# Kernel tuning notes

Hardware: AMD Instinct MI355X
Metric: run time of the kernel (lower is better)

## Reference

```python
import jax, jax.numpy as jnp
import numpy as np
from jax import lax

STRIDE, PAD, K = 1, 1, 3  # module defaults


def setup_inputs() -> dict:
    key = jax.random.key(0)
    k1, k2, k3, k4 = jax.random.split(key, 4)
    N, C, H, W, O = 8, 64, 112, 112, 64
    n = K * K
    x = jax.random.normal(k1, (N, C, H, W), jnp.float32)
    # kaiming-uniform-ish scale for main conv weight
    weight = jax.random.normal(k2, (O, C, K, K), jnp.float32) * (1.0 / np.sqrt(C * K * K))
    bias = jnp.zeros((O,), jnp.float32)
    # small random offset predictor (original zero-inits; small values exercise bilinear path)
    offset_w = jax.random.normal(k3, (3 * n, C, K, K), jnp.float32) * 0.01
    offset_b = jax.random.normal(k4, (3 * n,), jnp.float32) * 0.01
    return {"x": x, "weight": weight, "bias": bias, "offset_w": offset_w, "offset_b": offset_b}


def _bilinear(x, py, px):
    """Zero-padded bilinear sampling. x:[N,C,H,W]; py,px:[N,n,Ho,Wo] -> [N,C,n,Ho,Wo]."""
    N, C, H, W = x.shape
    xf = x.reshape(N, C, H * W)
    y0 = jnp.floor(py)
    x0 = jnp.floor(px)
    out = jnp.zeros((N, C) + py.shape[1:], x.dtype)
    for dy in (0.0, 1.0):
        for dx in (0.0, 1.0):
            yi = y0 + dy
            xi = x0 + dx
            w = (1.0 - jnp.abs(py - yi)) * (1.0 - jnp.abs(px - xi))
            valid = (yi >= 0) & (yi <= H - 1) & (xi >= 0) & (xi <= W - 1)
            yc = jnp.clip(yi, 0, H - 1).astype(jnp.int32)
            xc = jnp.clip(xi, 0, W - 1).astype(jnp.int32)
            idx = (yc * W + xc).reshape(N, 1, -1)
            g = jnp.take_along_axis(xf, jnp.broadcast_to(idx, (N, C, idx.shape[-1])), axis=2)
            g = g.reshape((N, C) + py.shape[1:])
            out = out + g * jnp.where(valid, w, 0.0)[:, None]
    return out


def reference(x, weight, bias, offset_w, offset_b):
    N, C, H, W = x.shape
    O = weight.shape[0]
    n = K * K
    # offset/mask predictor: 3x3 conv -> [N, 3*n, Ho, Wo]
    raw = lax.conv_general_dilated(
        x, offset_w, (STRIDE, STRIDE), [(PAD, PAD), (PAD, PAD)],
        dimension_numbers=("NCHW", "OIHW", "NCHW"),
    ) + offset_b[None, :, None, None]
    Ho, Wo = raw.shape[2], raw.shape[3]
    off = raw[:, : 2 * n].reshape(N, n, 2, Ho, Wo)       # (dy, dx) per tap
    mask = jax.nn.sigmoid(raw[:, 2 * n :])               # [N, n, Ho, Wo]
    # base sampling grid: p0 + kernel tap position
    tap_y = (jnp.arange(n) // K).astype(jnp.float32)[:, None, None]   # [n,1,1]
    tap_x = (jnp.arange(n) % K).astype(jnp.float32)[:, None, None]
    base_y = (jnp.arange(Ho) * STRIDE - PAD).astype(jnp.float32)[None, :, None] + tap_y  # [n,Ho,1]
    base_x = (jnp.arange(Wo) * STRIDE - PAD).astype(jnp.float32)[None, None, :] + tap_x  # [n,1,Wo]
    py = off[:, :, 0] + base_y[None]   # [N,n,Ho,Wo]
    px = off[:, :, 1] + base_x[None]
    sampled = _bilinear(x, py, px)                       # [N,C,n,Ho,Wo]
    val = sampled * mask[:, None]                        # modulation
    out = jnp.einsum("ncthw,oct->nohw", val, weight.reshape(O, C, n))
    return out + bias[None, :, None, None]
```

## Files before the change

kernel.cpp:

```cpp
#include <hip/hip_runtime.h>
#include <hip/hip_fp16.h>
#include <math.h>

#define NB  8
#define CIN 64
#define HH  112
#define WW  112
#define OC  64
#define HWSZ (HH*WW)
#define NPOS (NB*HWSZ)

#define PR 9
#define PC 21
#define NPOSP (PR*PC)
#define PATCH_CHUNKS (NPOSP*8)

#define TP_BLOCKS (HWSZ/64*NB)

typedef unsigned short u16;
typedef __attribute__((ext_vector_type(8))) _Float16 h8;
typedef __attribute__((ext_vector_type(4))) float floatx4;

#define XT_ELEMS   (NB*HWSZ*CIN)
#define WSWZ_ELEMS (18*4*64*8)
#define OSWZ_ELEMS (18*4*32*8)

union CV { uint4 u; h8 h; };

__device__ __forceinline__ u16 f2h(float f) { return __half_as_ushort(__float2half(f)); }
__device__ __forceinline__ __half2 H2(unsigned v) { union { unsigned u; __half2 h; } c; c.u = v; return c.h; }
__device__ __forceinline__ unsigned U2(__half2 h) { union { unsigned u; __half2 h; } c; c.h = h; return c.u; }
__device__ __forceinline__ unsigned pkh(float lo, float hi) {
    union { __half2 h; unsigned u; } c;
    c.h = __floats2half2_rn(lo, hi);
    return c.u;
}

struct TapW { __half2 w00, w01, w10, w11; };

__global__ __launch_bounds__(256) void prep_k(
    const float* __restrict__ x, const float* __restrict__ wgt,
    const float* __restrict__ offw,
    u16* __restrict__ xt, u16* __restrict__ wswz, u16* __restrict__ oswz)
{
    __shared__ float t[64][65];
    const int tid = threadIdx.x;
    const int bid = blockIdx.x;
    if (bid < TP_BLOCKS) {
        const int n   = bid & 7;
        const int hw0 = (bid >> 3) * 64;
        const int wv  = tid & 63;
        const int g   = tid >> 6;
        #pragma unroll
        for (int i = 0; i < 16; ++i) {
            const int c = i*4 + g;
            t[c][wv] = x[((size_t)n*CIN + c)*HWSZ + hw0 + wv];
        }
        __syncthreads();
        #pragma unroll
        for (int i = 0; i < 4; ++i) {
            const int unit = i*256 + tid;
            const int cg = unit & 15;
            const int hw = unit >> 4;
            uint2 o;
            o.x = pkh(t[cg*4+0][hw], t[cg*4+1][hw]);
            o.y = pkh(t[cg*4+2][hw], t[cg*4+3][hw]);
            *(uint2*)(xt + ((size_t)n*HWSZ + hw0 + hw)*CIN + cg*4) = o;
        }
    } else {
        const int gid = (bid - TP_BLOCKS)*256 + tid;
        if (gid < WSWZ_ELEMS) {
            const int j = gid & 7, o = (gid >> 3) & 63, q = (gid >> 9) & 3, s = gid >> 11;
            const int k = s*32 + q*8 + j;
            const int c = k & 63, tt = k >> 6;
            wswz[gid] = f2h(wgt[o*576 + c*9 + tt]);
        } else {
            const int g2 = gid - WSWZ_ELEMS;
            const int j = g2 & 7, r = (g2 >> 3) & 31, q = (g2 >> 8) & 3, s = g2 >> 10;
            const int k = s*32 + q*8 + j;
            const int c = k & 63, tt = k >> 6;
            oswz[g2] = (r < 27) ? f2h(offw[r*576 + c*9 + tt]) : (u16)0;
        }
    }
}

#define IML(DST, S_) { \
    const int t_ = (S_) >> 1; \
    const int ty_ = t_/3, tx_ = t_ - 3*ty_; \
    const int r_ = wid + 1 + ty_; \
    const int c_ = m + 1 + tx_; \
    const int pos_ = r_*PC + c_; \
    const int ck_ = ((S_) & 1)*4 + q; \
    DST = *(const uint4*)(patch + pos_*128 + ((ck_ ^ (pos_ & 7)) << 4)); }

#define OFF_MFMA(SRC, S_) { CV cb_; cb_.u = (SRC); \
    const u16* ap_ = oswz + ((S_)*4 + q)*256 + m*8; \
    acc0 = __builtin_amdgcn_mfma_f32_16x16x32_f16(*(const h8*)(ap_),       cb_.h, acc0, 0, 0, 0); \
    acc1 = __builtin_amdgcn_mfma_f32_16x16x32_f16(*(const h8*)(ap_ + 128), cb_.h, acc1, 0, 0, 0); }

#define HALF_STEP(R00, R01, R10, R11, TW, S_) { \
    CV cb_; \
    cb_.u.x = U2(__hfma2(H2((R00).x),(TW).w00, __hfma2(H2((R01).x),(TW).w01, \
              __hfma2(H2((R10).x),(TW).w10, __hmul2(H2((R11).x),(TW).w11))))); \
    cb_.u.y = U2(__hfma2(H2((R00).y),(TW).w00, __hfma2(H2((R01).y),(TW).w01, \
              __hfma2(H2((R10).y),(TW).w10, __hmul2(H2((R11).y),(TW).w11))))); \
    cb_.u.z = U2(__hfma2(H2((R00).z),(TW).w00, __hfma2(H2((R01).z),(TW).w01, \
              __hfma2(H2((R10).z),(TW).w10, __hmul2(H2((R11).z),(TW).w11))))); \
    cb_.u.w = U2(__hfma2(H2((R00).w),(TW).w00, __hfma2(H2((R01).w),(TW).w01, \
              __hfma2(H2((R10).w),(TW).w10, __hmul2(H2((R11).w),(TW).w11))))); \
    const u16* wp_ = wswz + ((S_)*4 + q)*512 + m*8; \
    acc[0] = __builtin_amdgcn_mfma_f32_16x16x32_f16(*(const h8*)(wp_),       cb_.h, acc[0], 0, 0, 0); \
    acc[1] = __builtin_amdgcn_mfma_f32_16x16x32_f16(*(const h8*)(wp_ + 128), cb_.h, acc[1], 0, 0, 0); \
    acc[2] = __builtin_amdgcn_mfma_f32_16x16x32_f16(*(const h8*)(wp_ + 256), cb_.h, acc[2], 0, 0, 0); \
    acc[3] = __builtin_amdgcn_mfma_f32_16x16x32_f16(*(const h8*)(wp_ + 384), cb_.h, acc[3], 0, 0, 0); }

#define UNPACK_TW(TW, WX, WY) { \
    (TW).w00 = __half2half2(__ushort_as_half((u16)((WX) & 0xFFFFu))); \
    (TW).w01 = __half2half2(__ushort_as_half((u16)((WX) >> 16))); \
    (TW).w10 = __half2half2(__ushort_as_half((u16)((WY) & 0xFFFFu))); \
    (TW).w11 = __half2half2(__ushort_as_half((u16)((WY) >> 16))); }

__global__ __launch_bounds__(256)
__attribute__((amdgpu_waves_per_eu(5, 8)))
void dcn_k(
    const u16*  __restrict__ xt,
    const u16*  __restrict__ wswz,
    const u16*  __restrict__ oswz,
    const float* __restrict__ bias,
    const float* __restrict__ offb,
    float* __restrict__ out)
{
    __shared__ uint4 patch4[PATCH_CHUNKS];
    __shared__ float rawsm[4][32][16];
    char* patch = (char*)patch4;
    unsigned* prmO = (unsigned*)rawsm;
    uint2*    prmW = (uint2*)((char*)rawsm + 2304);

    const int tid  = threadIdx.x;
    const int lane = tid & 63;
    const int wid  = tid >> 6;
    const int m    = lane & 15;
    const int q    = lane >> 4;

    const int n   = blockIdx.x & 7;
    const int idx = blockIdx.x >> 3;
    const int rg  = idx / 7;
    const int cc  = idx - rg*7;
    const int hoB = rg * 4;
    const int wo0 = cc * 16;
    const int ho  = hoB + wid;
    const u16* xtn = xt + (size_t)n * HWSZ * CIN;

    #pragma unroll
    for (int i = 0; i < 6; ++i) {
        const int u = i*256 + tid;
        if (u < PATCH_CHUNKS) {
            const int pos = u >> 3, ck = u & 7;
            const int pry = pos / PC;
            const int pcx = pos - pry*PC;
            const int gy = hoB - 2 + pry;
            const int gx = wo0 - 2 + pcx;
            uint4 v = {0u,0u,0u,0u};
            if (((unsigned)gy < HH) && ((unsigned)gx < WW))
                v = *(const uint4*)(xtn + (gy*WW + gx)*CIN + ck*8);
            *(uint4*)(patch + pos*128 + ((ck ^ (pos & 7)) << 4)) = v;
        }
    }
    __syncthreads();

    {
        uint4 b[6];
        floatx4 acc0 = {0.f,0.f,0.f,0.f}, acc1 = {0.f,0.f,0.f,0.f};
        #pragma unroll
        for (int s = 0; s < 6; ++s) IML(b[s], s)
        #pragma unroll
        for (int s = 0; s < 6; ++s) {
            uint4 nv; IML(nv, s + 6)
            OFF_MFMA(b[s], s)
            b[s] = nv;
        }
        #pragma unroll
        for (int s = 0; s < 6; ++s) {
            uint4 nv; IML(nv, s + 12)
            OFF_MFMA(b[s], s + 6)
            b[s] = nv;
        }
        #pragma unroll
        for (int s = 0; s < 6; ++s) OFF_MFMA(b[s], s + 12)

        #pragma unroll
        for (int r = 0; r < 4; ++r) {
            rawsm[wid][q*4 + r][m]      = acc0[r];
            rawsm[wid][16 + q*4 + r][m] = acc1[r];
        }
    }
    __syncthreads();

    float vy[3], vx[3], vmk[3];
    #pragma unroll
    for (int i = 0; i < 3; ++i) {
        const int e = i*64 + lane;
        if (e < 144) {
            const int t = e >> 4, p = e & 15;
            vy[i]  = rawsm[wid][2*t][p];
            vx[i]  = rawsm[wid][2*t + 1][p];
            vmk[i] = rawsm[wid][18 + t][p];
        }
    }
    __syncthreads();
    #pragma unroll
    for (int i = 0; i < 3; ++i) {
        const int e = i*64 + lane;
        if (e < 144) {
            const int t = e >> 4;
            const int p = e & 15;
            const int ty = t / 3, tx = t - 3*ty;
            const float py = vy[i] + offb[2*t]     + (float)(ho - 1 + ty);
            const float px = vx[i] + offb[2*t + 1] + (float)(wo0 + p - 1 + tx);
            const float mk = 1.f / (1.f + expf(-(vmk[i] + offb[18 + t])));
            const float y0f = floorf(py), x0f = floorf(px);
            const float fy = py - y0f, fx = px - x0f;
            const int y0 = (int)y0f, x0 = (int)x0f;
            const float gy = 1.f - fy, gx = 1.f - fx;
            const bool vy0 = (unsigned)y0       < HH;
            const bool vy1 = (unsigned)(y0 + 1) < HH;
            const bool vx0 = (unsigned)x0       < WW;
            const bool vx1 = (unsigned)(x0 + 1) < WW;
            const float w00 = (vy0 && vx0) ? gy*gx*mk : 0.f;
            const float w01 = (vy0 && vx1) ? gy*fx*mk : 0.f;
            const float w10 = (vy1 && vx0) ? fy*gx*mk : 0.f;
            const float w11 = (vy1 && vx1) ? fy*fx*mk : 0.f;
            const int yc0 = min(max(y0, 0), HH-1),  yc1 = min(max(y0+1, 0), HH-1);
            const int xc0 = min(max(x0, 0), WW-1),  xc1 = min(max(x0+1, 0), WW-1);
            const unsigned o00 = (unsigned)((yc0*WW + xc0)*CIN);
            const unsigned dxb = (unsigned)(xc1 - xc0);
            const unsigned dyb = (unsigned)(yc1 - yc0);
            const int r0  = yc0 - (hoB - 2);
            const int c0l = xc0 - (wo0 - 2);
            const bool inp = (r0 >= 0) && (r0 + (int)dyb <= PR-1)
                          && (c0l >= 0) && (c0l + (int)dxb <= PC-1);
            const int pos00 = r0*PC + c0l;
            prmO[(wid*9 + t)*16 + p] = o00 | (dxb << 20) | (dyb << 21)
                            | (((unsigned)pos00 & 0xFFu) << 22)
                            | (inp ? (1u << 30) : 0u);
            uint2 Wv;
            Wv.x = (unsigned)__half_as_ushort(__float2half(w00))
                 | ((unsigned)__half_as_ushort(__float2half(w01)) << 16);
            Wv.y = (unsigned)__half_as_ushort(__float2half(w10))
                 | ((unsigned)__half_as_ushort(__float2half(w11)) << 16);
            prmW[(wid*9 + t)*16 + p] = Wv;
        }
    }
    __syncthreads();

    floatx4 acc[4];
    #pragma unroll
    for (int i = 0; i < 4; ++i) acc[i] = (floatx4){0.f,0.f,0.f,0.f};

    const unsigned* PoB = prmO + wid*144 + m;
    const uint2*    PwB = prmW + wid*144 + m;

    unsigned band = 0xFFFFFFFFu;
    #pragma unroll
    for (int t = 0; t < 9; ++t) band &= PoB[t*16];

    if (__all((int)((band >> 30) & 1u))) {
        unsigned Po = PoB[0];
        uint2    Pw = PwB[0];
        #pragma unroll
        for (int t = 0; t < 9; ++t) {
            const unsigned PoN = (t < 8) ? PoB[(t+1)*16] : 0u;
            const uint2    PwN = (t < 8) ? PwB[(t+1)*16] : Pw;
            const int p00 = (int)((Po >> 22) & 0xFFu);
            const int dxb = (int)((Po >> 20) & 1u);
            const int dyb = (int)((Po >> 21) & 1u);
            const int p01 = p00 + dxb;
            const int p10 = p00 + dyb*PC;
            const int p11 = p10 + dxb;
            const int a00 = p00*128 + ((q ^ (p00 & 7)) << 4);
            const int a01 = p01*128 + ((q ^ (p01 & 7)) << 4);
            const int a10 = p10*128 + ((q ^ (p10 & 7)) << 4);
            const int a11 = p11*128 + ((q ^ (p11 & 7)) << 4);
            const uint4 g0 = *(const uint4*)(patch + a00);
            const uint4 g1 = *(const uint4*)(patch + a01);
            const uint4 g2 = *(const uint4*)(patch + a10);
            const uint4 g3 = *(const uint4*)(patch + a11);
            const uint4 g4 = *(const uint4*)(patch + (a00 ^ 64));
            const uint4 g5 = *(const uint4*)(patch + (a01 ^ 64));
            const uint4 g6 = *(const uint4*)(patch + (a10 ^ 64));
            const uint4 g7 = *(const uint4*)(patch + (a11 ^ 64));
            TapW tw; UNPACK_TW(tw, Pw.x, Pw.y)
            HALF_STEP(g0, g1, g2, g3, tw, 2*t)
            HALF_STEP(g4, g5, g6, g7, tw, 2*t + 1)
            Po = PoN; Pw = PwN;
        }
    } else {
        const int ch0 = q*8, ch1 = 32 + q*8;
        #pragma unroll
        for (int t = 0; t < 9; ++t) {
            const unsigned Po = PoB[t*16];
            const uint2    Pw = PwB[t*16];
            TapW tw; UNPACK_TW(tw, Pw.x, Pw.y)
            uint4 g0,g1,g2,g3,g4,g5,g6,g7;
            if (__all((int)((Po >> 30) & 1u))) {
                const int p00 = (int)((Po >> 22) & 0xFFu);
                const int dxb = (int)((Po >> 20) & 1u);
                const int dyb = (int)((Po >> 21) & 1u);
                const int p01 = p00 + dxb;
                const int p10 = p00 + dyb*PC;
                const int p11 = p10 + dxb;
                const int a00 = p00*128 + ((q ^ (p00 & 7)) << 4);
                const int a01 = p01*128 + ((q ^ (p01 & 7)) << 4);
                const int a10 = p10*128 + ((q ^ (p10 & 7)) << 4);
                const int a11 = p11*128 + ((q ^ (p11 & 7)) << 4);
                g0 = *(const uint4*)(patch + a00);
                g1 = *(const uint4*)(patch + a01);
                g2 = *(const uint4*)(patch + a10);
                g3 = *(const uint4*)(patch + a11);
                g4 = *(const uint4*)(patch + (a00 ^ 64));
                g5 = *(const uint4*)(patch + (a01 ^ 64));
                g6 = *(const uint4*)(patch + (a10 ^ 64));
                g7 = *(const uint4*)(patch + (a11 ^ 64));
            } else {
                const int o00 = (int)(Po & 0xFFFFFu);
                const int dx  = (int)((Po >> 20) & 1u) << 6;
                const int dy  = (int)((Po >> 21) & 1u) * (WW*CIN);
                g0 = *(const uint4*)(xtn + o00 + ch0);
                g1 = *(const uint4*)(xtn + o00 + dx + ch0);
                g2 = *(const uint4*)(xtn + o00 + dy + ch0);
                g3 = *(const uint4*)(xtn + o00 + dx + dy + ch0);
                g4 = *(const uint4*)(xtn + o00 + ch1);
                g5 = *(const uint4*)(xtn + o00 + dx + ch1);
                g6 = *(const uint4*)(xtn + o00 + dy + ch1);
                g7 = *(const uint4*)(xtn + o00 + dx + dy + ch1);
            }
            HALF_STEP(g0, g1, g2, g3, tw, 2*t)
            HALF_STEP(g4, g5, g6, g7, tw, 2*t + 1)
        }
    }

    #pragma unroll
    for (int ob = 0; ob < 4; ++ob) {
        #pragma unroll
        for (int r = 0; r < 4; ++r) {
            const int o = ob*16 + q*4 + r;
            out[(((size_t)n*OC + o)*HH + ho)*WW + wo0 + m] = acc[ob][r] + bias[o];
        }
    }
}

extern "C" void kernel_launch(void* const* d_in, const int* in_sizes, int n_in,
                              void* d_out, int out_size, void* d_ws, size_t ws_size,
                              hipStream_t stream)
{
    const float* x    = (const float*)d_in[0];
    const float* wgt  = (const float*)d_in[1];
    const float* bias = (const float*)d_in[2];
    const float* offw = (const float*)d_in[3];
    const float* offb = (const float*)d_in[4];
    float* out = (float*)d_out;

    u16* xt   = (u16*)d_ws;
    u16* wswz = xt + XT_ELEMS;
    u16* oswz = wswz + WSWZ_ELEMS;

    prep_k<<<dim3(TP_BLOCKS + (WSWZ_ELEMS + OSWZ_ELEMS)/256), 256, 0, stream>>>(
        x, wgt, offw, xt, wswz, oswz);
    dcn_k<<<dim3(NPOS/64), 256, 0, stream>>>(xt, wswz, oswz, bias, offb, out);
}
```

Measured before the change: 115.2 us.

## Split channel reduction across two wave groups with 512-thread blocks

```diff
diff --git a/kernel.cpp b/kernel.cpp
--- a/kernel.cpp
+++ b/kernel.cpp
@@ -87,7 +87,7 @@
 #define IML(DST, S_) { \
     const int t_ = (S_) >> 1; \
     const int ty_ = t_/3, tx_ = t_ - 3*ty_; \
-    const int r_ = wid + 1 + ty_; \
+    const int r_ = row + 1 + ty_; \
     const int c_ = m + 1 + tx_; \
     const int pos_ = r_*PC + c_; \
     const int ck_ = ((S_) & 1)*4 + q; \
@@ -120,8 +120,8 @@
     (TW).w10 = __half2half2(__ushort_as_half((u16)((WY) & 0xFFFFu))); \
     (TW).w11 = __half2half2(__ushort_as_half((u16)((WY) >> 16))); }
 
-__global__ __launch_bounds__(256)
-__attribute__((amdgpu_waves_per_eu(5, 8)))
+__global__ __launch_bounds__(512)
+__attribute__((amdgpu_waves_per_eu(8)))
 void dcn_k(
     const u16*  __restrict__ xt,
     const u16*  __restrict__ wswz,
@@ -132,13 +132,15 @@
 {
     __shared__ uint4 patch4[PATCH_CHUNKS];
     __shared__ float rawsm[4][32][16];
+    __shared__ unsigned prmO[4][9][16];
+    __shared__ uint2    prmW[4][9][16];
     char* patch = (char*)patch4;
-    unsigned* prmO = (unsigned*)rawsm;
-    uint2*    prmW = (uint2*)((char*)rawsm + 2304);
 
     const int tid  = threadIdx.x;
     const int lane = tid & 63;
     const int wid  = tid >> 6;
+    const int row  = wid & 3;
+    const int h    = wid >> 2;
     const int m    = lane & 15;
     const int q    = lane >> 4;
 
@@ -148,12 +150,12 @@
     const int cc  = idx - rg*7;
     const int hoB = rg * 4;
     const int wo0 = cc * 16;
-    const int ho  = hoB + wid;
+    const int ho  = hoB + row;
     const u16* xtn = xt + (size_t)n * HWSZ * CIN;
 
     #pragma unroll
-    for (int i = 0; i < 6; ++i) {
-        const int u = i*256 + tid;
+    for (int i = 0; i < 3; ++i) {
+        const int u = i*512 + tid;
         if (u < PATCH_CHUNKS) {
             const int pos = u >> 3, ck = u & 7;
             const int pry = pos / PC;
@@ -169,87 +171,76 @@
     __syncthreads();
 
     {
-        uint4 b[6];
+        uint4 b[3];
         floatx4 acc0 = {0.f,0.f,0.f,0.f}, acc1 = {0.f,0.f,0.f,0.f};
-        #pragma unroll
-        for (int s = 0; s < 6; ++s) IML(b[s], s)
-        #pragma unroll
-        for (int s = 0; s < 6; ++s) {
-            uint4 nv; IML(nv, s + 6)
-            OFF_MFMA(b[s], s)
-            b[s] = nv;
-        }
-        #pragma unroll
-        for (int s = 0; s < 6; ++s) {
-            uint4 nv; IML(nv, s + 12)
-            OFF_MFMA(b[s], s + 6)
-            b[s] = nv;
-        }
-        #pragma unroll
-        for (int s = 0; s < 6; ++s) OFF_MFMA(b[s], s + 12)
-
-        #pragma unroll
-        for (int r = 0; r < 4; ++r) {
-            rawsm[wid][q*4 + r][m]      = acc0[r];
-            rawsm[wid][16 + q*4 + r][m] = acc1[r];
-        }
-    }
-    __syncthreads();
-
-    float vy[3], vx[3], vmk[3];
-    #pragma unroll
-    for (int i = 0; i < 3; ++i) {
-        const int e = i*64 + lane;
-        if (e < 144) {
-            const int t = e >> 4, p = e & 15;
-            vy[i]  = rawsm[wid][2*t][p];
-            vx[i]  = rawsm[wid][2*t + 1][p];
-            vmk[i] = rawsm[wid][18 + t][p];
-        }
-    }
-    __syncthreads();
-    #pragma unroll
-    for (int i = 0; i < 3; ++i) {
-        const int e = i*64 + lane;
-        if (e < 144) {
-            const int t = e >> 4;
-            const int p = e & 15;
-            const int ty = t / 3, tx = t - 3*ty;
-            const float py = vy[i] + offb[2*t]     + (float)(ho - 1 + ty);
-            const float px = vx[i] + offb[2*t + 1] + (float)(wo0 + p - 1 + tx);
-            const float mk = 1.f / (1.f + expf(-(vmk[i] + offb[18 + t])));
-            const float y0f = floorf(py), x0f = floorf(px);
-            const float fy = py - y0f, fx = px - x0f;
-            const int y0 = (int)y0f, x0 = (int)x0f;
-            const float gy = 1.f - fy, gx = 1.f - fx;
-            const bool vy0 = (unsigned)y0       < HH;
-            const bool vy1 = (unsigned)(y0 + 1) < HH;
-            const bool vx0 = (unsigned)x0       < WW;
-            const bool vx1 = (unsigned)(x0 + 1) < WW;
-            const float w00 = (vy0 && vx0) ? gy*gx*mk : 0.f;
-            const float w01 = (vy0 && vx1) ? gy*fx*mk : 0.f;
-            const float w10 = (vy1 && vx0) ? fy*gx*mk : 0.f;
-            const float w11 = (vy1 && vx1) ? fy*fx*mk : 0.f;
-            const int yc0 = min(max(y0, 0), HH-1),  yc1 = min(max(y0+1, 0), HH-1);
-            const int xc0 = min(max(x0, 0), WW-1),  xc1 = min(max(x0+1, 0), WW-1);
-            const unsigned o00 = (unsigned)((yc0*WW + xc0)*CIN);
-            const unsigned dxb = (unsigned)(xc1 - xc0);
-            const unsigned dyb = (unsigned)(yc1 - yc0);
-            const int r0  = yc0 - (hoB - 2);
-            const int c0l = xc0 - (wo0 - 2);
-            const bool inp = (r0 >= 0) && (r0 + (int)dyb <= PR-1)
-                          && (c0l >= 0) && (c0l + (int)dxb <= PC-1);
-            const int pos00 = r0*PC + c0l;
-            prmO[(wid*9 + t)*16 + p] = o00 | (dxb << 20) | (dyb << 21)
-                            | (((unsigned)pos00 & 0xFFu) << 22)
-                            | (inp ? (1u << 30) : 0u);
-            uint2 Wv;
-            Wv.x = (unsigned)__half_as_ushort(__float2half(w00))
-                 | ((unsigned)__half_as_ushort(__float2half(w01)) << 16);
-            Wv.y = (unsigned)__half_as_ushort(__float2half(w10))
-                 | ((unsigned)__half_as_ushort(__float2half(w11)) << 16);
-            prmW[(wid*9 + t)*16 + p] = Wv;
-        }
+        IML(b[0], 0 + h) IML(b[1], 2 + h) IML(b[2], 4 + h)
+        #pragma unroll
+        for (int t = 0; t < 9; ++t) {
+            uint4 nv;
+            if (t < 6) IML(nv, 2*(t+3) + h)
+            OFF_MFMA(b[t%3], 2*t + h)
+            if (t < 6) b[t%3] = nv;
+        }
+        if (h == 0) {
+            #pragma unroll
+            for (int r = 0; r < 4; ++r) {
+                rawsm[row][q*4 + r][m]      = acc0[r];
+                rawsm[row][16 + q*4 + r][m] = acc1[r];
+            }
+        }
+        __syncthreads();
+        if (h == 1) {
+            #pragma unroll
+            for (int r = 0; r < 4; ++r) {
+                rawsm[row][q*4 + r][m]      += acc0[r];
+                rawsm[row][16 + q*4 + r][m] += acc1[r];
+            }
+        }
+        __syncthreads();
+    }
+
+    auto tapParam = [&](int t, int p) {
+        const int ty = t / 3, tx = t - 3*ty;
+        const float py = rawsm[row][2*t][p]     + offb[2*t]     + (float)(ho - 1 + ty);
+        const float px = rawsm[row][2*t + 1][p] + offb[2*t + 1] + (float)(wo0 + p - 1 + tx);
+        const float mk = 1.f / (1.f + expf(-(rawsm[row][18 + t][p] + offb[18 + t])));
+        const float y0f = floorf(py), x0f = floorf(px);
+        const float fy = py - y0f, fx = px - x0f;
+        const int y0 = (int)y0f, x0 = (int)x0f;
+        const float gy = 1.f - fy, gx = 1.f - fx;
+        const bool vy0 = (unsigned)y0       < HH;
+        const bool vy1 = (unsigned)(y0 + 1) < HH;
+        const bool vx0 = (unsigned)x0       < WW;
+        const bool vx1 = (unsigned)(x0 + 1) < WW;
+        const float w00 = (vy0 && vx0) ? gy*gx*mk : 0.f;
+        const float w01 = (vy0 && vx1) ? gy*fx*mk : 0.f;
+        const float w10 = (vy1 && vx0) ? fy*gx*mk : 0.f;
+        const float w11 = (vy1 && vx1) ? fy*fx*mk : 0.f;
+        const int yc0 = min(max(y0, 0), HH-1),  yc1 = min(max(y0+1, 0), HH-1);
+        const int xc0 = min(max(x0, 0), WW-1),  xc1 = min(max(x0+1, 0), WW-1);
+        const unsigned o00 = (unsigned)((yc0*WW + xc0)*CIN);
+        const unsigned dxb = (unsigned)(xc1 - xc0);
+        const unsigned dyb = (unsigned)(yc1 - yc0);
+        const int r0  = yc0 - (hoB - 2);
+        const int c0l = xc0 - (wo0 - 2);
+        const bool inp = (r0 >= 0) && (r0 + (int)dyb <= PR-1)
+                      && (c0l >= 0) && (c0l + (int)dxb <= PC-1);
+        const int pos00 = r0*PC + c0l;
+        prmO[row][t][p] = o00 | (dxb << 20) | (dyb << 21)
+                        | (((unsigned)pos00 & 0xFFu) << 22)
+                        | (inp ? (1u << 30) : 0u);
+        uint2 Wv;
+        Wv.x = (unsigned)__half_as_ushort(__float2half(w00))
+             | ((unsigned)__half_as_ushort(__float2half(w01)) << 16);
+        Wv.y = (unsigned)__half_as_ushort(__float2half(w10))
+             | ((unsigned)__half_as_ushort(__float2half(w11)) << 16);
+        prmW[row][t][p] = Wv;
+    };
+    if (h == 0) {
+        tapParam(lane >> 4, lane & 15);
+        if (lane < 16) tapParam(4, lane & 15);
+    } else {
+        tapParam(5 + (lane >> 4), lane & 15);
     }
     __syncthreads();
 
@@ -257,51 +248,42 @@
     #pragma unroll
     for (int i = 0; i < 4; ++i) acc[i] = (floatx4){0.f,0.f,0.f,0.f};
 
-    const unsigned* PoB = prmO + wid*144 + m;
-    const uint2*    PwB = prmW + wid*144 + m;
+    const int hx = h << 6;
 
     unsigned band = 0xFFFFFFFFu;
     #pragma unroll
-    for (int t = 0; t < 9; ++t) band &= PoB[t*16];
+    for (int t = 0; t < 9; ++t) band &= prmO[row][t][m];
 
     if (__all((int)((band >> 30) & 1u))) {
-        unsigned Po = PoB[0];
-        uint2    Pw = PwB[0];
         #pragma unroll
         for (int t = 0; t < 9; ++t) {
-            const unsigned PoN = (t < 8) ? PoB[(t+1)*16] : 0u;
-            const uint2    PwN = (t < 8) ? PwB[(t+1)*16] : Pw;
+            const unsigned Po = prmO[row][t][m];
+            const uint2    Pw = prmW[row][t][m];
             const int p00 = (int)((Po >> 22) & 0xFFu);
             const int dxb = (int)((Po >> 20) & 1u);
             const int dyb = (int)((Po >> 21) & 1u);
             const int p01 = p00 + dxb;
             const int p10 = p00 + dyb*PC;
             const int p11 = p10 + dxb;
-            const int a00 = p00*128 + ((q ^ (p00 & 7)) << 4);
-            const int a01 = p01*128 + ((q ^ (p01 & 7)) << 4);
-            const int a10 = p10*128 + ((q ^ (p10 & 7)) << 4);
-            const int a11 = p11*128 + ((q ^ (p11 & 7)) << 4);
+            const int a00 = (p00*128 + ((q ^ (p00 & 7)) << 4)) ^ hx;
+            const int a01 = (p01*128 + ((q ^ (p01 & 7)) << 4)) ^ hx;
+            const int a10 = (p10*128 + ((q ^ (p10 & 7)) << 4)) ^ hx;
+            const int a11 = (p11*128 + ((q ^ (p11 & 7)) << 4)) ^ hx;
             const uint4 g0 = *(const uint4*)(patch + a00);
             const uint4 g1 = *(const uint4*)(patch + a01);
             const uint4 g2 = *(const uint4*)(patch + a10);
             const uint4 g3 = *(const uint4*)(patch + a11);
-            const uint4 g4 = *(const uint4*)(patch + (a00 ^ 64));
-            const uint4 g5 = *(const uint4*)(patch + (a01 ^ 64));
-            const uint4 g6 = *(const uint4*)(patch + (a10 ^ 64));
-            const uint4 g7 = *(const uint4*)(patch + (a11 ^ 64));
             TapW tw; UNPACK_TW(tw, Pw.x, Pw.y)
-            HALF_STEP(g0, g1, g2, g3, tw, 2*t)
-            HALF_STEP(g4, g5, g6, g7, tw, 2*t + 1)
-            Po = PoN; Pw = PwN;
+            HALF_STEP(g0, g1, g2, g3, tw, 2*t + h)
         }
     } else {
-        const int ch0 = q*8, ch1 = 32 + q*8;
+        const int ch = h*32 + q*8;
         #pragma unroll
         for (int t = 0; t < 9; ++t) {
-            const unsigned Po = PoB[t*16];
-            const uint2    Pw = PwB[t*16];
+            const unsigned Po = prmO[row][t][m];
+            const uint2    Pw = prmW[row][t][m];
             TapW tw; UNPACK_TW(tw, Pw.x, Pw.y)
-            uint4 g0,g1,g2,g3,g4,g5,g6,g7;
+            uint4 g0,g1,g2,g3;
             if (__all((int)((Po >> 30) & 1u))) {
                 const int p00 = (int)((Po >> 22) & 0xFFu);
                 const int dxb = (int)((Po >> 20) & 1u);
@@ -309,38 +291,46 @@
                 const int p01 = p00 + dxb;
                 const int p10 = p00 + dyb*PC;
                 const int p11 = p10 + dxb;
-                const int a00 = p00*128 + ((q ^ (p00 & 7)) << 4);
-                const int a01 = p01*128 + ((q ^ (p01 & 7)) << 4);
-                const int a10 = p10*128 + ((q ^ (p10 & 7)) << 4);
-                const int a11 = p11*128 + ((q ^ (p11 & 7)) << 4);
-                g0 = *(const uint4*)(patch + a00);
-                g1 = *(const uint4*)(patch + a01);
-                g2 = *(const uint4*)(patch + a10);
-                g3 = *(const uint4*)(patch + a11);
-                g4 = *(const uint4*)(patch + (a00 ^ 64));
-                g5 = *(const uint4*)(patch + (a01 ^ 64));
-                g6 = *(const uint4*)(patch + (a10 ^ 64));
-                g7 = *(const uint4*)(patch + (a11 ^ 64));
+                g0 = *(const uint4*)(patch + ((p00*128 + ((q ^ (p00 & 7)) << 4)) ^ hx));
+                g1 = *(const uint4*)(patch + ((p01*128 + ((q ^ (p01 & 7)) << 4)) ^ hx));
+                g2 = *(const uint4*)(patch + ((p10*128 + ((q ^ (p10 & 7)) << 4)) ^ hx));
+                g3 = *(const uint4*)(patch + ((p11*128 + ((q ^ (p11 & 7)) << 4)) ^ hx));
             } else {
                 const int o00 = (int)(Po & 0xFFFFFu);
                 const int dx  = (int)((Po >> 20) & 1u) << 6;
                 const int dy  = (int)((Po >> 21) & 1u) * (WW*CIN);
-                g0 = *(const uint4*)(xtn + o00 + ch0);
-                g1 = *(const uint4*)(xtn + o00 + dx + ch0);
-                g2 = *(const uint4*)(xtn + o00 + dy + ch0);
-                g3 = *(const uint4*)(xtn + o00 + dx + dy + ch0);
-                g4 = *(const uint4*)(xtn + o00 + ch1);
-                g5 = *(const uint4*)(xtn + o00 + dx + ch1);
-                g6 = *(const uint4*)(xtn + o00 + dy + ch1);
-                g7 = *(const uint4*)(xtn + o00 + dx + dy + ch1);
+                g0 = *(const uint4*)(xtn + o00 + ch);
+                g1 = *(const uint4*)(xtn + o00 + dx + ch);
+                g2 = *(const uint4*)(xtn + o00 + dy + ch);
+                g3 = *(const uint4*)(xtn + o00 + dx + dy + ch);
             }
-            HALF_STEP(g0, g1, g2, g3, tw, 2*t)
-            HALF_STEP(g4, g5, g6, g7, tw, 2*t + 1)
-        }
-    }
-
+            HALF_STEP(g0, g1, g2, g3, tw, 2*t + h)
+        }
+    }
+
+    __syncthreads();
+    uint4* accq = (uint4*)patch4;
+    {
+        const int wbase = ((row*2 + h)*2)*64 + lane;
+        if (h == 0) {
+            accq[wbase]      = *(uint4*)&acc[2];
+            accq[wbase + 64] = *(uint4*)&acc[3];
+        } else {
+            accq[wbase]      = *(uint4*)&acc[0];
+            accq[wbase + 64] = *(uint4*)&acc[1];
+        }
+    }
+    __syncthreads();
+    {
+        const int pb = ((row*2 + (h ^ 1))*2)*64 + lane;
+        const floatx4 o0 = *(const floatx4*)&accq[pb];
+        const floatx4 o1 = *(const floatx4*)&accq[pb + 64];
+        if (h == 0) { acc[0] += o0; acc[1] += o1; }
+        else        { acc[2] += o0; acc[3] += o1; }
+    }
     #pragma unroll
-    for (int ob = 0; ob < 4; ++ob) {
+    for (int j = 0; j < 2; ++j) {
+        const int ob = h*2 + j;
         #pragma unroll
         for (int r = 0; r < 4; ++r) {
             const int o = ob*16 + q*4 + r;
@@ -366,5 +356,5 @@
 
     prep_k<<<dim3(TP_BLOCKS + (WSWZ_ELEMS + OSWZ_ELEMS)/256), 256, 0, stream>>>(
         x, wgt, offw, xt, wswz, oswz);
-    dcn_k<<<dim3(NPOS/64), 256, 0, stream>>>(xt, wswz, oswz, bias, offb, out);
+    dcn_k<<<dim3(NPOS/64), 512, 0, stream>>>(xt, wswz, oswz, bias, offb, out);
 }
```

Result: slower. 144.5 us (+25.4%).
